# Performance work log

Hardware: AMD Instinct MI355X
Metric: run time of the kernel (lower is better)

Reference implementation:

```python
import jax, jax.numpy as jnp
import numpy as np


def setup_inputs() -> dict:
    key = jax.random.key(0)
    ks = jax.random.split(key, 7)
    E = 768; CH = 3; PS = 16; B = 128; P = 196
    return {
        "x": jax.random.normal(ks[0], (B, P, E), dtype=jnp.float32),
        "We": jax.random.normal(ks[1], (CH * PS * PS, E), dtype=jnp.float32) * (1.0 / np.sqrt(E)),
        "be": jax.random.normal(ks[2], (CH * PS * PS,), dtype=jnp.float32) * 0.01,
        "filter_re": jax.random.normal(ks[3], (1, 1, 1, PS, PS), dtype=jnp.float32),
        "filter_im": jax.random.normal(ks[4], (1, 1, 1, PS, PS), dtype=jnp.float32),
        "Wd": jax.random.normal(ks[5], (E, CH * PS * PS), dtype=jnp.float32) * (1.0 / np.sqrt(CH * PS * PS)),
        "bd": jax.random.normal(ks[6], (E,), dtype=jnp.float32) * 0.01,
        "ch": 3,
        "patch_size": 16,
    }


def reference(x, We, be, filter_re, filter_im, Wd, bd, ch, patch_size):
    # encode: [b,p,E] -> [b,p,ch*ps*ps]
    h = jnp.einsum('bpe,ce->bpc', x, We) + be
    b, p, _ = h.shape
    h = h.reshape(b, p, ch, patch_size, patch_size)
    # batched 2D FFT over the two trailing patch dims
    hf = jnp.fft.fft2(h, axes=(-2, -1))
    filt = (filter_re + 1j * filter_im).astype(hf.dtype)  # [1,1,1,ps,ps]
    r = jnp.fft.ifft2(hf * filt, axes=(-2, -1))
    a = jnp.abs(r).reshape(b, p, ch * patch_size * patch_size)
    # decode: [b,p,ch*ps*ps] -> [b,p,E]
    return jnp.einsum('bpc,ec->bpe', a, Wd) + bd
```

## Files before the change

kernel.cpp:

```cpp
#include <hip/hip_runtime.h>

typedef short short8 __attribute__((ext_vector_type(8)));
typedef unsigned short ushort8 __attribute__((ext_vector_type(8)));
typedef float f32x4 __attribute__((ext_vector_type(4)));

__device__ __forceinline__ unsigned short f32_to_bf16(float f) {
  unsigned u = __float_as_uint(f);
  unsigned r = 0x7fffu + ((u >> 16) & 1u);
  return (unsigned short)((u + r) >> 16);
}
__device__ __forceinline__ float bf16_to_f32(unsigned short h) {
  return __uint_as_float(((unsigned)h) << 16);
}

__global__ void cvt_f32_bf16(const float* __restrict__ s,
                             unsigned short* __restrict__ d, int n8) {
  int i = blockIdx.x * blockDim.x + threadIdx.x;
  if (i >= n8) return;
  const float4* sp = (const float4*)s;
  float4 a = sp[2 * i], b = sp[2 * i + 1];
  ushort8 o;
  o[0] = f32_to_bf16(a.x); o[1] = f32_to_bf16(a.y);
  o[2] = f32_to_bf16(a.z); o[3] = f32_to_bf16(a.w);
  o[4] = f32_to_bf16(b.x); o[5] = f32_to_bf16(b.y);
  o[6] = f32_to_bf16(b.z); o[7] = f32_to_bf16(b.w);
  ((ushort8*)d)[i] = o;
}

__device__ __forceinline__ void gload_lds16(const void* g, void* l) {
  auto* gp = (const __attribute__((address_space(1))) uint32_t*)((uintptr_t)g);
  auto* lp = (__attribute__((address_space(3))) uint32_t*)(uint32_t)(uintptr_t)l;
  __builtin_amdgcn_global_load_lds(gp, lp, 16, 0, 0);
}

constexpr float C16T[16] = {
    1.f,  0.9238795325112867f,  0.7071067811865476f,  0.3826834323650898f,
    0.f, -0.3826834323650898f, -0.7071067811865476f, -0.9238795325112867f,
   -1.f, -0.9238795325112867f, -0.7071067811865476f, -0.3826834323650898f,
    0.f,  0.3826834323650898f,  0.7071067811865476f,  0.9238795325112867f};
constexpr float S16T[16] = {
    0.f,  0.3826834323650898f,  0.7071067811865476f,  0.9238795325112867f,
    1.f,  0.9238795325112867f,  0.7071067811865476f,  0.3826834323650898f,
    0.f, -0.3826834323650898f, -0.7071067811865476f, -0.9238795325112867f,
   -1.f, -0.9238795325112867f, -0.7071067811865476f, -0.3826834323650898f};

__device__ __forceinline__ void dft16(const float* xr, const float* xi,
                                      float* Xr, float* Xi, const float sgn) {
  float Tr[4][4], Ti[4][4];
#pragma unroll
  for (int c0 = 0; c0 < 4; ++c0) {
    float ar = xr[c0],      ai = xi[c0];
    float br = xr[c0 + 4],  bi = xi[c0 + 4];
    float cr = xr[c0 + 8],  ci = xi[c0 + 8];
    float dr = xr[c0 + 12], di = xi[c0 + 12];
    float Er = ar + cr, Ei = ai + ci, Fr = ar - cr, Fi = ai - ci;
    float Gr = br + dr, Gi = bi + di, Hr = br - dr, Hi = bi - di;
    Tr[c0][0] = Er + Gr; Ti[c0][0] = Ei + Gi;
    Tr[c0][2] = Er - Gr; Ti[c0][2] = Ei - Gi;
    float wHr = -sgn * Hi, wHi = sgn * Hr;
    Tr[c0][1] = Fr + wHr; Ti[c0][1] = Fi + wHi;
    Tr[c0][3] = Fr - wHr; Ti[c0][3] = Fi - wHi;
  }
#pragma unroll
  for (int u = 0; u < 16; ++u) {
    const int m = u & 3;
    float sr = Tr[0][m], si = Ti[0][m];
#pragma unroll
    for (int c0 = 1; c0 < 4; ++c0) {
      const int k = (u * c0) & 15;
      const float wr = C16T[k];
      const float wi = sgn * S16T[k];
      sr += wr * Tr[c0][m] - wi * Ti[c0][m];
      si += wr * Ti[c0][m] + wi * Tr[c0][m];
    }
    Xr[u] = sr; Xi[u] = si;
  }
}

__global__ __launch_bounds__(256) void fold_filter(
    const float* __restrict__ We, const float* __restrict__ be,
    const float* __restrict__ fre, const float* __restrict__ fim,
    unsigned short* __restrict__ Bpp, float* __restrict__ be_re,
    float* __restrict__ be_im) {
  __shared__ float2 S[16 * 276];
  const int tid = threadIdx.x;
  const int p = tid >> 4;
  const int q = tid & 15;
  const int item = blockIdx.x * 16 + p;
  const bool isW = item < 2304;
  const bool isB = (item >= 2304) && (item < 2307);
  const int e = isW ? (item / 3) : 0;
  const int ch = isW ? (item % 3) : (isB ? (item - 2304) : 0);
  const int sb = p * 276;

  {
    float xr[16], xi[16], Xr[16], Xi[16];
#pragma unroll
    for (int c = 0; c < 16; ++c) {
      const int crow = ch * 256 + q * 16 + c;
      xr[c] = isW ? We[(size_t)crow * 768 + e] : be[crow];
      xi[c] = 0.f;
    }
    dft16(xr, xi, Xr, Xi, -1.f);
#pragma unroll
    for (int u = 0; u < 16; ++u) S[sb + q * 17 + u] = make_float2(Xr[u], Xi[u]);
  }
  __syncthreads();

  {
    float xr[16], xi[16], Xr[16], Xi[16];
#pragma unroll
    for (int k = 0; k < 16; ++k) {
      float2 t = S[sb + k * 17 + q];
      xr[k] = t.x; xi[k] = t.y;
    }
    dft16(xr, xi, Xr, Xi, -1.f);
#pragma unroll
    for (int v = 0; v < 16; ++v) {
      float fr = fre[v * 16 + q], fi = fim[v * 16 + q];
      float tr = Xr[v] * fr - Xi[v] * fi;
      float ti = Xr[v] * fi + Xi[v] * fr;
      xr[v] = tr; xi[v] = ti;
    }
    dft16(xr, xi, Xr, Xi, 1.f);
#pragma unroll
    for (int r = 0; r < 16; ++r) S[sb + r * 17 + q] = make_float2(Xr[r], Xi[r]);
  }
  __syncthreads();

  {
    float xr[16], xi[16], Xr[16], Xi[16];
#pragma unroll
    for (int u = 0; u < 16; ++u) {
      float2 t = S[sb + q * 17 + u];
      xr[u] = t.x; xi[u] = t.y;
    }
    dft16(xr, xi, Xr, Xi, 1.f);
#pragma unroll
    for (int c = 0; c < 16; ++c) {
      const int crow = ch * 256 + q * 16 + c;
      const float rr = Xr[c] * (1.f / 256.f);
      const float ri = Xi[c] * (1.f / 256.f);
      if (isW) {
        const size_t rre = (size_t)(crow >> 5) * 64 + (crow & 31);
        Bpp[(rre)*768 + e]      = f32_to_bf16(rr);
        Bpp[(rre + 32)*768 + e] = f32_to_bf16(ri);
      } else if (isB) {
        be_re[crow] = rr;
        be_im[crow] = ri;
      }
    }
  }
}

__global__ __launch_bounds__(256) void gemm_enc(
    const unsigned short* __restrict__ A, const unsigned short* __restrict__ B,
    const float* __restrict__ be_re, const float* __restrict__ be_im,
    unsigned short* __restrict__ out, int M, int K, int nbx) {
  __shared__ __align__(16) unsigned short As[2][128 * 64];
  __shared__ __align__(16) unsigned short Bs[2][128 * 64];

  const int tid = threadIdx.x;
  const int lane = tid & 63;
  const int wid = tid >> 6;
  const int wr = wid >> 1, wc = wid & 1;

  const int nwg = gridDim.x;
  const int cpx = nwg >> 3;
  const int bid = blockIdx.x;
  const int lid = (bid & 7) * cpx + (bid >> 3);
  const int m0 = (lid / nbx) * 128, n0 = (lid % nbx) * 128;

  const int lr8 = lane >> 3;
  const int swk = ((lane & 7) ^ lr8) * 8;

  f32x4 acc[4][4] = {};

  auto STAGE = [&](int buf, int k0) {
#pragma unroll
    for (int c = 0; c < 4; ++c) {
      const int rowc = wid * 32 + c * 8;
      gload_lds16(A + (size_t)(m0 + rowc + lr8) * K + (k0 + swk),
                  &As[buf][rowc * 64]);
      gload_lds16(B + (size_t)(n0 + rowc + lr8) * K + (k0 + swk),
                  &Bs[buf][rowc * 64]);
    }
  };

  const int rsel = lane & 15;
  auto COMPUTE = [&](int buf) {
#pragma unroll
    for (int ks = 0; ks < 2; ++ks) {
      const int kbyte = ks * 64 + (lane >> 4) * 16;
      short8 af[4], bf[4];
#pragma unroll
      for (int m = 0; m < 4; ++m) {
        const int row = wr * 64 + m * 16 + rsel;
        af[m] = *(const short8*)((const char*)&As[buf][0] +
                                 row * 128 + (kbyte ^ ((row & 7) << 4)));
      }
#pragma unroll
      for (int n = 0; n < 4; ++n) {
        const int row = wc * 64 + n * 16 + rsel;
        bf[n] = *(const short8*)((const char*)&Bs[buf][0] +
                                 row * 128 + (kbyte ^ ((row & 7) << 4)));
      }
#pragma unroll
      for (int m = 0; m < 4; ++m)
#pragma unroll
        for (int n = 0; n < 4; ++n)
          acc[m][n] = __builtin_amdgcn_mfma_f32_16x16x32_bf16(
              af[m], bf[n], acc[m][n], 0, 0, 0);
    }
  };

  const int nk = K >> 6;
  STAGE(0, 0);
  __syncthreads();
  int cur = 0;
  for (int t = 1; t < nk; ++t) {
    STAGE(cur ^ 1, t * 64);
    COMPUTE(cur);
    __syncthreads();
    cur ^= 1;
  }
  COMPUTE(cur);

  const int fr = lane & 15, fq = lane >> 4;
  const int cbase = (n0 + wc * 64) >> 1;
#pragma unroll
  for (int n = 0; n < 2; ++n) {
    const int gcol = cbase + n * 16 + fr;
    const float br = be_re[gcol], bi = be_im[gcol];
#pragma unroll
    for (int m = 0; m < 4; ++m) {
      const int grow = m0 + wr * 64 + m * 16 + fq * 4;
#pragma unroll
      for (int j = 0; j < 4; ++j) {
        const float re = acc[m][n][j] + br;
        const float im = acc[m][n + 2][j] + bi;
        out[(size_t)(grow + j) * 768 + gcol] =
            f32_to_bf16(sqrtf(re * re + im * im));
      }
    }
  }
}

__global__ __launch_bounds__(256) void gemm_bt(
    const unsigned short* __restrict__ A, const unsigned short* __restrict__ B,
    const float* __restrict__ bias, float* __restrict__ out,
    int M, int N, int K, int nbx) {
  __shared__ __align__(16) unsigned short As[2][128 * 64];
  __shared__ __align__(16) unsigned short Bs[2][128 * 64];

  const int tid = threadIdx.x;
  const int lane = tid & 63;
  const int wid = tid >> 6;
  const int wr = wid >> 1, wc = wid & 1;

  const int nwg = gridDim.x;
  const int cpx = nwg >> 3;
  const int bid = blockIdx.x;
  const int lid = (bid & 7) * cpx + (bid >> 3);
  const int m0 = (lid / nbx) * 128, n0 = (lid % nbx) * 128;

  const int lr8 = lane >> 3;
  const int swk = ((lane & 7) ^ lr8) * 8;

  f32x4 acc[4][4] = {};

  auto STAGE = [&](int buf, int k0) {
#pragma unroll
    for (int c = 0; c < 4; ++c) {
      const int rowc = wid * 32 + c * 8;
      gload_lds16(A + (size_t)(m0 + rowc + lr8) * K + (k0 + swk),
                  &As[buf][rowc * 64]);
      gload_lds16(B + (size_t)(n0 + rowc + lr8) * K + (k0 + swk),
                  &Bs[buf][rowc * 64]);
    }
  };

  const int rsel = lane & 15;
  auto COMPUTE = [&](int buf) {
#pragma unroll
    for (int ks = 0; ks < 2; ++ks) {
      const int kbyte = ks * 64 + (lane >> 4) * 16;
      short8 af[4], bf[4];
#pragma unroll
      for (int m = 0; m < 4; ++m) {
        const int row = wr * 64 + m * 16 + rsel;
        af[m] = *(const short8*)((const char*)&As[buf][0] +
                                 row * 128 + (kbyte ^ ((row & 7) << 4)));
      }
#pragma unroll
      for (int n = 0; n < 4; ++n) {
        const int row = wc * 64 + n * 16 + rsel;
        bf[n] = *(const short8*)((const char*)&Bs[buf][0] +
                                 row * 128 + (kbyte ^ ((row & 7) << 4)));
      }
#pragma unroll
      for (int m = 0; m < 4; ++m)
#pragma unroll
        for (int n = 0; n < 4; ++n)
          acc[m][n] = __builtin_amdgcn_mfma_f32_16x16x32_bf16(
              af[m], bf[n], acc[m][n], 0, 0, 0);
    }
  };

  const int nk = K >> 6;
  STAGE(0, 0);
  __syncthreads();
  int cur = 0;
  for (int t = 1; t < nk; ++t) {
    STAGE(cur ^ 1, t * 64);
    COMPUTE(cur);
    __syncthreads();
    cur ^= 1;
  }
  COMPUTE(cur);

  const int fr = lane & 15, fq = lane >> 4;
#pragma unroll
  for (int n = 0; n < 4; ++n) {
    const int gcol = n0 + wc * 64 + n * 16 + fr;
    const float bv = bias[gcol];
#pragma unroll
    for (int m = 0; m < 4; ++m) {
      const int grow = m0 + wr * 64 + m * 16 + fq * 4;
#pragma unroll
      for (int j = 0; j < 4; ++j)
        out[(size_t)(grow + j) * N + gcol] = acc[m][n][j] + bv;
    }
  }
}

extern "C" void kernel_launch(void* const* d_in, const int* in_sizes, int n_in,
                              void* d_out, int out_size, void* d_ws,
                              size_t ws_size, hipStream_t stream) {
  const float* x   = (const float*)d_in[0];
  const float* We  = (const float*)d_in[1];
  const float* be  = (const float*)d_in[2];
  const float* fre = (const float*)d_in[3];
  const float* fim = (const float*)d_in[4];
  const float* Wd  = (const float*)d_in[5];
  const float* bd  = (const float*)d_in[6];

  const int E = 768, C = 768;
  const int nX = in_sizes[0];
  const int M  = nX / E;
  const int nW = E * C;

  char* w = (char*)d_ws;
  unsigned short* xb    = (unsigned short*)w;
  unsigned short* Wdb   = (unsigned short*)(w + (size_t)nX * 2);
  unsigned short* Bpp   = Wdb + nW;
  float*          be_re = (float*)(Bpp + 2 * (size_t)nW);
  float*          be_im = be_re + C;
  unsigned short* hb    = (unsigned short*)(be_im + C);

  cvt_f32_bf16<<<(nX / 8 + 255) / 256, 256, 0, stream>>>(x, xb, nX / 8);
  cvt_f32_bf16<<<(nW / 8 + 255) / 256, 256, 0, stream>>>(Wd, Wdb, nW / 8);

  fold_filter<<<145, 256, 0, stream>>>(We, be, fre, fim, Bpp, be_re, be_im);

  const int nbx1 = (2 * C) / 128;
  gemm_enc<<<nbx1 * (M / 128), 256, 0, stream>>>(xb, Bpp, be_re, be_im, hb, M,
                                                 E, nbx1);

  const int nbx2 = E / 128;
  gemm_bt<<<nbx2 * (M / 128), 256, 0, stream>>>(hb, Wdb, bd, (float*)d_out, M,
                                                E, C, nbx2);
}
```

Measured before the change: 152.3 us.

## Replace folded-filter encoder with separate circulant spectral GEMM stage

Drops the per-weight FFT folding of the filter into an expanded encoder weight matrix. Instead it builds a 256x256 circulant matrix (real and imaginary parts) from the inverse DFT of the filter, which is the spatial form of the circular convolution. It then runs three GEMMs: a plain encoder, a per-channel spectral GEMM with a magnitude epilogue, and the decoder. This cuts the encoder's doubled N dimension and the heavy fold kernel, but adds an intermediate bf16 round trip through memory and one more kernel launch.

```diff
diff --git a/kernel.cpp b/kernel.cpp
--- a/kernel.cpp
+++ b/kernel.cpp
@@ -8,9 +8,6 @@
   unsigned u = __float_as_uint(f);
   unsigned r = 0x7fffu + ((u >> 16) & 1u);
   return (unsigned short)((u + r) >> 16);
-}
-__device__ __forceinline__ float bf16_to_f32(unsigned short h) {
-  return __uint_as_float(((unsigned)h) << 16);
 }
 
 __global__ void cvt_f32_bf16(const float* __restrict__ s,
@@ -44,119 +41,42 @@
     0.f, -0.3826834323650898f, -0.7071067811865476f, -0.9238795325112867f,
    -1.f, -0.9238795325112867f, -0.7071067811865476f, -0.3826834323650898f};
 
-__device__ __forceinline__ void dft16(const float* xr, const float* xi,
-                                      float* Xr, float* Xi, const float sgn) {
-  float Tr[4][4], Ti[4][4];
-#pragma unroll
-  for (int c0 = 0; c0 < 4; ++c0) {
-    float ar = xr[c0],      ai = xi[c0];
-    float br = xr[c0 + 4],  bi = xi[c0 + 4];
-    float cr = xr[c0 + 8],  ci = xi[c0 + 8];
-    float dr = xr[c0 + 12], di = xi[c0 + 12];
-    float Er = ar + cr, Ei = ai + ci, Fr = ar - cr, Fi = ai - ci;
-    float Gr = br + dr, Gi = bi + di, Hr = br - dr, Hi = bi - di;
-    Tr[c0][0] = Er + Gr; Ti[c0][0] = Ei + Gi;
-    Tr[c0][2] = Er - Gr; Ti[c0][2] = Ei - Gi;
-    float wHr = -sgn * Hi, wHi = sgn * Hr;
-    Tr[c0][1] = Fr + wHr; Ti[c0][1] = Fi + wHi;
-    Tr[c0][3] = Fr - wHr; Ti[c0][3] = Fi - wHi;
-  }
-#pragma unroll
-  for (int u = 0; u < 16; ++u) {
-    const int m = u & 3;
-    float sr = Tr[0][m], si = Ti[0][m];
-#pragma unroll
-    for (int c0 = 1; c0 < 4; ++c0) {
-      const int k = (u * c0) & 15;
-      const float wr = C16T[k];
-      const float wi = sgn * S16T[k];
-      sr += wr * Tr[c0][m] - wi * Ti[c0][m];
-      si += wr * Ti[c0][m] + wi * Tr[c0][m];
-    }
-    Xr[u] = sr; Xi[u] = si;
-  }
-}
-
-__global__ __launch_bounds__(256) void fold_filter(
-    const float* __restrict__ We, const float* __restrict__ be,
+__global__ __launch_bounds__(256) void build_gpp(
     const float* __restrict__ fre, const float* __restrict__ fim,
-    unsigned short* __restrict__ Bpp, float* __restrict__ be_re,
-    float* __restrict__ be_im) {
-  __shared__ float2 S[16 * 276];
-  const int tid = threadIdx.x;
-  const int p = tid >> 4;
-  const int q = tid & 15;
-  const int item = blockIdx.x * 16 + p;
-  const bool isW = item < 2304;
-  const bool isB = (item >= 2304) && (item < 2307);
-  const int e = isW ? (item / 3) : 0;
-  const int ch = isW ? (item % 3) : (isB ? (item - 2304) : 0);
-  const int sb = p * 276;
-
-  {
-    float xr[16], xi[16], Xr[16], Xi[16];
-#pragma unroll
-    for (int c = 0; c < 16; ++c) {
-      const int crow = ch * 256 + q * 16 + c;
-      xr[c] = isW ? We[(size_t)crow * 768 + e] : be[crow];
-      xi[c] = 0.f;
-    }
-    dft16(xr, xi, Xr, Xi, -1.f);
-#pragma unroll
-    for (int u = 0; u < 16; ++u) S[sb + q * 17 + u] = make_float2(Xr[u], Xi[u]);
-  }
+    unsigned short* __restrict__ Gpp) {
+  __shared__ float Gr[256], Gi[256];
+  const int t = threadIdx.x;
+  const int d1 = t >> 4, d2 = t & 15;
+  float sr = 0.f, si = 0.f;
+#pragma unroll
+  for (int v1 = 0; v1 < 16; ++v1) {
+    const int k1 = (v1 * d1) & 15;
+#pragma unroll
+    for (int v2 = 0; v2 < 16; ++v2) {
+      const int k = (k1 + v2 * d2) & 15;
+      const float c = C16T[k], s = S16T[k];
+      const float a = fre[v1 * 16 + v2], b = fim[v1 * 16 + v2];
+      sr += a * c - b * s;
+      si += a * s + b * c;
+    }
+  }
+  Gr[t] = sr * (1.f / 256.f);
+  Gi[t] = si * (1.f / 256.f);
   __syncthreads();
-
-  {
-    float xr[16], xi[16], Xr[16], Xi[16];
-#pragma unroll
-    for (int k = 0; k < 16; ++k) {
-      float2 t = S[sb + k * 17 + q];
-      xr[k] = t.x; xi[k] = t.y;
-    }
-    dft16(xr, xi, Xr, Xi, -1.f);
-#pragma unroll
-    for (int v = 0; v < 16; ++v) {
-      float fr = fre[v * 16 + q], fi = fim[v * 16 + q];
-      float tr = Xr[v] * fr - Xi[v] * fi;
-      float ti = Xr[v] * fi + Xi[v] * fr;
-      xr[v] = tr; xi[v] = ti;
-    }
-    dft16(xr, xi, Xr, Xi, 1.f);
-#pragma unroll
-    for (int r = 0; r < 16; ++r) S[sb + r * 17 + q] = make_float2(Xr[r], Xi[r]);
-  }
-  __syncthreads();
-
-  {
-    float xr[16], xi[16], Xr[16], Xi[16];
-#pragma unroll
-    for (int u = 0; u < 16; ++u) {
-      float2 t = S[sb + q * 17 + u];
-      xr[u] = t.x; xi[u] = t.y;
-    }
-    dft16(xr, xi, Xr, Xi, 1.f);
-#pragma unroll
-    for (int c = 0; c < 16; ++c) {
-      const int crow = ch * 256 + q * 16 + c;
-      const float rr = Xr[c] * (1.f / 256.f);
-      const float ri = Xi[c] * (1.f / 256.f);
-      if (isW) {
-        const size_t rre = (size_t)(crow >> 5) * 64 + (crow & 31);
-        Bpp[(rre)*768 + e]      = f32_to_bf16(rr);
-        Bpp[(rre + 32)*768 + e] = f32_to_bf16(ri);
-      } else if (isB) {
-        be_re[crow] = rr;
-        be_im[crow] = ri;
-      }
-    }
-  }
-}
-
-__global__ __launch_bounds__(256) void gemm_enc(
+  const int p = blockIdx.x;
+  const int p1 = p >> 4, p2 = p & 15;
+  const size_t rre = (size_t)(p >> 5) * 64 + (p & 31);
+  const int q1 = t >> 4, q2 = t & 15;
+  const int idx = (((p1 - q1) & 15) << 4) | ((p2 - q2) & 15);
+  Gpp[rre * 256 + t] = f32_to_bf16(Gr[idx]);
+  Gpp[(rre + 32) * 256 + t] = f32_to_bf16(Gi[idx]);
+}
+
+template <int OUT_BF16>
+__global__ __launch_bounds__(256) void gemm_bt(
     const unsigned short* __restrict__ A, const unsigned short* __restrict__ B,
-    const float* __restrict__ be_re, const float* __restrict__ be_im,
-    unsigned short* __restrict__ out, int M, int K, int nbx) {
+    const float* __restrict__ bias, void* __restrict__ out,
+    int M, int N, int K, int nbx) {
   __shared__ __align__(16) unsigned short As[2][128 * 64];
   __shared__ __align__(16) unsigned short Bs[2][128 * 64];
 
@@ -227,32 +147,32 @@
   COMPUTE(cur);
 
   const int fr = lane & 15, fq = lane >> 4;
-  const int cbase = (n0 + wc * 64) >> 1;
-#pragma unroll
-  for (int n = 0; n < 2; ++n) {
-    const int gcol = cbase + n * 16 + fr;
-    const float br = be_re[gcol], bi = be_im[gcol];
+#pragma unroll
+  for (int n = 0; n < 4; ++n) {
+    const int gcol = n0 + wc * 64 + n * 16 + fr;
+    const float bv = bias[gcol];
 #pragma unroll
     for (int m = 0; m < 4; ++m) {
       const int grow = m0 + wr * 64 + m * 16 + fq * 4;
 #pragma unroll
       for (int j = 0; j < 4; ++j) {
-        const float re = acc[m][n][j] + br;
-        const float im = acc[m][n + 2][j] + bi;
-        out[(size_t)(grow + j) * 768 + gcol] =
-            f32_to_bf16(sqrtf(re * re + im * im));
-      }
-    }
-  }
-}
-
-__global__ __launch_bounds__(256) void gemm_bt(
+        const float v = acc[m][n][j] + bv;
+        if (OUT_BF16)
+          ((unsigned short*)out)[(size_t)(grow + j) * N + gcol] = f32_to_bf16(v);
+        else
+          ((float*)out)[(size_t)(grow + j) * N + gcol] = v;
+      }
+    }
+  }
+}
+
+__global__ __launch_bounds__(256) void gemm_spec(
     const unsigned short* __restrict__ A, const unsigned short* __restrict__ B,
-    const float* __restrict__ bias, float* __restrict__ out,
-    int M, int N, int K, int nbx) {
+    unsigned short* __restrict__ out, int M2, int nbx) {
   __shared__ __align__(16) unsigned short As[2][128 * 64];
   __shared__ __align__(16) unsigned short Bs[2][128 * 64];
 
+  const int K = 256;
   const int tid = threadIdx.x;
   const int lane = tid & 63;
   const int wid = tid >> 6;
@@ -320,16 +240,20 @@
   COMPUTE(cur);
 
   const int fr = lane & 15, fq = lane >> 4;
-#pragma unroll
-  for (int n = 0; n < 4; ++n) {
-    const int gcol = n0 + wc * 64 + n * 16 + fr;
-    const float bv = bias[gcol];
+  const int cbase = (n0 + wc * 64) >> 1;
+#pragma unroll
+  for (int n = 0; n < 2; ++n) {
+    const int gcol = cbase + n * 16 + fr;
 #pragma unroll
     for (int m = 0; m < 4; ++m) {
       const int grow = m0 + wr * 64 + m * 16 + fq * 4;
 #pragma unroll
-      for (int j = 0; j < 4; ++j)
-        out[(size_t)(grow + j) * N + gcol] = acc[m][n][j] + bv;
+      for (int j = 0; j < 4; ++j) {
+        const float re = acc[m][n][j];
+        const float im = acc[m][n + 2][j];
+        out[(size_t)(grow + j) * 256 + gcol] =
+            f32_to_bf16(sqrtf(re * re + im * im));
+      }
     }
   }
 }
@@ -351,23 +275,23 @@
   const int nW = E * C;
 
   char* w = (char*)d_ws;
-  unsigned short* xb    = (unsigned short*)w;
-  unsigned short* Wdb   = (unsigned short*)(w + (size_t)nX * 2);
-  unsigned short* Bpp   = Wdb + nW;
-  float*          be_re = (float*)(Bpp + 2 * (size_t)nW);
-  float*          be_im = be_re + C;
-  unsigned short* hb    = (unsigned short*)(be_im + C);
+  unsigned short* xb  = (unsigned short*)w;
+  unsigned short* Web = (unsigned short*)(w + (size_t)nX * 2);
+  unsigned short* Wdb = Web + nW;
+  unsigned short* Gpp = Wdb + nW;
+  unsigned short* hb  = Gpp + 512 * 256;
 
   cvt_f32_bf16<<<(nX / 8 + 255) / 256, 256, 0, stream>>>(x, xb, nX / 8);
+  cvt_f32_bf16<<<(nW / 8 + 255) / 256, 256, 0, stream>>>(We, Web, nW / 8);
   cvt_f32_bf16<<<(nW / 8 + 255) / 256, 256, 0, stream>>>(Wd, Wdb, nW / 8);
 
-  fold_filter<<<145, 256, 0, stream>>>(We, be, fre, fim, Bpp, be_re, be_im);
-
-  const int nbx1 = (2 * C) / 128;
-  gemm_enc<<<nbx1 * (M / 128), 256, 0, stream>>>(xb, Bpp, be_re, be_im, hb, M,
-                                                 E, nbx1);
-
-  const int nbx2 = E / 128;
-  gemm_bt<<<nbx2 * (M / 128), 256, 0, stream>>>(hb, Wdb, bd, (float*)d_out, M,
-                                                E, C, nbx2);
-}
+  build_gpp<<<256, 256, 0, stream>>>(fre, fim, Gpp);
+
+  gemm_bt<1><<<6 * (M / 128), 256, 0, stream>>>(xb, Web, be, hb, M, C, E, 6);
+
+  const int M2 = M * 3;
+  gemm_spec<<<4 * (M2 / 128), 256, 0, stream>>>(hb, Gpp, xb, M2, 4);
+
+  gemm_bt<0><<<6 * (M / 128), 256, 0, stream>>>(xb, Wdb, bd, (float*)d_out, M,
+                                                E, C, 6);
+}
```

Measured after the change: 153.7 us. No clear change (+0.9%).
